# Optimization experiments

Hardware: AMD Instinct MI355X
Metric: run time of the kernel (lower is better)

Reference implementation:

```python
import jax, jax.numpy as jnp
import numpy as np
from jax import lax

N = 16384
K = 16
EPS = 1e-5


def setup_inputs() -> dict:
    key = jax.random.key(0)
    ks = jax.random.split(key, 10)

    def w(k, shape):
        fan_in = shape[0]
        return jax.random.normal(k, shape, jnp.float32) / np.sqrt(fan_in)

    return {
        "pos": jax.random.normal(ks[0], (N, 3), jnp.float32),
        "normal": jax.random.normal(ks[1], (N, 3), jnp.float32),
        # conv1 mlp: Linear(9,64) -> GroupNorm(8,64) -> ReLU -> Linear(64,64)
        "W1a": w(ks[2], (9, 64)), "b1a": jnp.zeros((64,), jnp.float32),
        "g1": jnp.ones((64,), jnp.float32), "beta1": jnp.zeros((64,), jnp.float32),
        "W1b": w(ks[3], (64, 64)), "b1b": jnp.zeros((64,), jnp.float32),
        # conv2 mlp: Linear(67,64) -> GroupNorm(8,64) -> ReLU -> Linear(64,64)
        "W2a": w(ks[4], (67, 64)), "b2a": jnp.zeros((64,), jnp.float32),
        "g2": jnp.ones((64,), jnp.float32), "beta2": jnp.zeros((64,), jnp.float32),
        "W2b": w(ks[5], (64, 64)), "b2b": jnp.zeros((64,), jnp.float32),
        # conv3 mlp: Linear(67,128) -> GroupNorm(16,128) -> ReLU -> Linear(128,128)
        "W3a": w(ks[6], (67, 128)), "b3a": jnp.zeros((128,), jnp.float32),
        "g3": jnp.ones((128,), jnp.float32), "beta3": jnp.zeros((128,), jnp.float32),
        "W3b": w(ks[7], (128, 128)), "b3b": jnp.zeros((128,), jnp.float32),
    }


def knn_graph(pos, k):
    # [N,N] squared distances; loop=True -> self is included (distance 0).
    sq = jnp.sum(pos * pos, axis=1)
    d2 = sq[:, None] + sq[None, :] - 2.0 * (pos @ pos.T)
    _, nbr = lax.top_k(-d2, k)  # [N,k] neighbor (source) indices per target node
    return nbr


def group_norm(h, gamma, beta, groups):
    # h: [N,k,C]; normalize each group of channels per edge sample.
    n, k, c = h.shape
    hg = h.reshape(n, k, groups, c // groups)
    mu = hg.mean(axis=-1, keepdims=True)
    var = hg.var(axis=-1, keepdims=True)
    hg = (hg - mu) * lax.rsqrt(var + EPS)
    return hg.reshape(n, k, c) * gamma + beta


def pointnet_conv(x, pos, nbr, Wa, ba, gamma, beta, Wb, bb, groups):
    # message: concat(x_j, pos_j - pos_i), MLP per edge, max-aggregate over neighbors
    xj = x[nbr]                              # [N,k,C_in]
    rel = pos[nbr] - pos[:, None, :]         # [N,k,3]
    m = jnp.concatenate([xj, rel], axis=-1)  # [N,k,C_in+3]
    h = m @ Wa + ba
    h = jax.nn.relu(group_norm(h, gamma, beta, groups))
    h = h @ Wb + bb
    return jnp.max(h, axis=1)                # [N,C_out]


def reference(pos, normal, W1a, b1a, g1, beta1, W1b, b1b,
              W2a, b2a, g2, beta2, W2b, b2b,
              W3a, b3a, g3, beta3, W3b, b3b):
    nbr = knn_graph(pos, K)
    h = jnp.concatenate([pos, normal], axis=-1)  # [N,6]
    h1 = jax.nn.relu(pointnet_conv(h, pos, nbr, W1a, b1a, g1, beta1, W1b, b1b, 8))
    h2 = jax.nn.relu(pointnet_conv(h1, pos, nbr, W2a, b2a, g2, beta2, W2b, b2b, 8))
    h3 = jax.nn.relu(pointnet_conv(h2, pos, nbr, W3a, b3a, g3, beta3, W3b, b3b, 16))
    return (h1, h2, h3)
```

## Files before the change

kernel.cpp:

```cpp
#include <hip/hip_runtime.h>
#include <hip/hip_bf16.h>
#include <stdint.h>

typedef unsigned long long u64;
typedef unsigned int u32;
typedef __attribute__((ext_vector_type(8))) short bf16x8;
typedef __attribute__((ext_vector_type(4))) float f32x4;

__device__ __forceinline__ float ldv(const void* p, size_t idx, int mode) {
  return mode ? __bfloat162float(((const __hip_bfloat16*)p)[idx])
              : ((const float*)p)[idx];
}
__device__ __forceinline__ void stv(void* p, size_t idx, int mode, float v) {
  if (mode) ((__hip_bfloat16*)p)[idx] = __float2bfloat16(v);
  else      ((float*)p)[idx] = v;
}
__device__ __forceinline__ unsigned short f2bfb(float f) {
  u32 u = __float_as_uint(f);
  u32 r = u + 0x7fffu + ((u >> 16) & 1u);
  return (unsigned short)(r >> 16);
}
__device__ __forceinline__ u64 shfl64(u64 v, int src) {
  int lo = __shfl((int)(u32)(v & 0xffffffffu), src, 64);
  int hi = __shfl((int)(u32)(v >> 32), src, 64);
  return ((u64)(u32)hi << 32) | (u32)lo;
}
__device__ __forceinline__ u64 shflxor64(u64 v, int m) {
  int lo = __shfl_xor((int)(u32)(v & 0xffffffffu), m, 64);
  int hi = __shfl_xor((int)(u32)(v >> 32), m, 64);
  return ((u64)(u32)hi << 32) | (u32)lo;
}
__device__ __forceinline__ u64 shfl64w16(u64 v, int src) {
  int lo = __shfl((int)(u32)(v & 0xffffffffu), src, 16);
  int hi = __shfl((int)(u32)(v >> 32), src, 16);
  return ((u64)(u32)hi << 32) | (u32)lo;
}

__global__ void PointNetSimple_61409442398998_kernel() {}

struct CvtEnt { const void* src; float* dst; int n; };
struct CvtArgs { CvtEnt e[12]; };
struct WEnt { const void* src; unsigned short* dst; int K, N, Kpad; };
struct WArgs { WEnt e[6]; };

__global__ void setup_kernel(const void* __restrict__ pos,
                             const void* __restrict__ nrm,
                             WArgs wa, CvtArgs ca,
                             int* __restrict__ flag,
                             float4* __restrict__ pos4,
                             float* __restrict__ h0, int n) {
  const unsigned short* u16p = (const unsigned short*)pos;
  int cnt = 0;
  for (int k = 0; k < 32; ++k) {
    int e = (u16p[k] >> 7) & 0xff;
    if (e >= 110 && e <= 140) cnt++;
  }
  const int mode = (cnt >= 26) ? 1 : 0;

  const int nprep = n >> 8;
  const int b = blockIdx.x;
  if (b < nprep) {
    int i = b * 256 + threadIdx.x;
    float x = ldv(pos, 3*(size_t)i+0, mode);
    float y = ldv(pos, 3*(size_t)i+1, mode);
    float z = ldv(pos, 3*(size_t)i+2, mode);
    pos4[i] = make_float4(x, y, z, x*x + y*y + z*z);
    h0[6*(size_t)i+0] = x; h0[6*(size_t)i+1] = y; h0[6*(size_t)i+2] = z;
    h0[6*(size_t)i+3] = ldv(nrm, 3*(size_t)i+0, mode);
    h0[6*(size_t)i+4] = ldv(nrm, 3*(size_t)i+1, mode);
    h0[6*(size_t)i+5] = ldv(nrm, 3*(size_t)i+2, mode);
  } else {
    int r = b - nprep;
    if (r < 6) {
      WEnt ent = wa.e[r];
      for (int t = threadIdx.x; t < ent.N * ent.Kpad; t += blockDim.x) {
        int nn = t / ent.Kpad;
        int k  = t - nn * ent.Kpad;
        float v = (k < ent.K) ? ldv(ent.src, (size_t)k * ent.N + nn, mode) : 0.0f;
        ent.dst[t] = f2bfb(v);
      }
      if (r == 0 && threadIdx.x == 0) flag[0] = mode;
    } else {
      for (int t2 = 0; t2 < 12; ++t2) {
        CvtEnt ent = ca.e[t2];
        for (int t = threadIdx.x; t < ent.n; t += blockDim.x)
          ent.dst[t] = ldv(ent.src, t, mode);
      }
    }
  }
}

#define KNN_TPB 512
#define KNN_WPB 8
#define KNN_TPW 4
#define KCH 1024

__device__ __forceinline__ void knn_flush(u64* __restrict__ wbuf_t, int& cnt,
                                          u64& val, float& th, int lane) {
  u64 cand = (lane < cnt) ? wbuf_t[lane] : ~0ull;
#pragma unroll
  for (int k = 2; k <= 64; k <<= 1) {
#pragma unroll
    for (int j = k >> 1; j > 0; j >>= 1) {
      u64 other = shflxor64(cand, j);
      bool up    = ((lane & k) == 0) || (k == 64);
      bool lower = ((lane & j) == 0);
      bool keepMin = (up == lower);
      u64 mn = cand < other ? cand : other;
      u64 mx = cand < other ? other : cand;
      cand = keepMin ? mn : mx;
    }
  }
  u64 rev = shfl64w16(cand, 15 - (lane & 15));
  u64 lo = val < rev ? val : rev;
#pragma unroll
  for (int j = 8; j > 0; j >>= 1) {
    u64 other = shflxor64(lo, j);
    bool lower = ((lane & j) == 0);
    u64 mn = lo < other ? lo : other;
    u64 mx = lo < other ? other : lo;
    lo = lower ? mn : mx;
  }
  val = (lane < 16) ? lo : ~0ull;
  u64 t15 = shfl64(val, 15);
  th = __uint_as_float((u32)(t15 >> 32));
  cnt = 0;
}

__global__ __launch_bounds__(KNN_TPB) void knn6_kernel(
    const float4* __restrict__ pos4, int* __restrict__ nbr, int n) {
  __shared__ float4 sp[2][KCH];
  __shared__ u64 buf[KNN_WPB][KNN_TPW][64];
  const int tid  = threadIdx.x;
  const int lane = tid & 63;
  const int wid  = tid >> 6;
  const int tbase = (blockIdx.x * KNN_WPB + wid) * KNN_TPW;

  float4 pi[KNN_TPW];
  float  thr[KNN_TPW];
  u64    val[KNN_TPW];
  int    cnt[KNN_TPW];
#pragma unroll
  for (int tt = 0; tt < KNN_TPW; ++tt) {
    pi[tt]  = pos4[tbase + tt];
    thr[tt] = 3.4e38f;
    val[tt] = ~0ull;
    cnt[tt] = 0;
  }

  for (int t = tid; t < KCH; t += KNN_TPB) sp[0][t] = pos4[t];
  __syncthreads();

  const int nch = n / KCH;
  for (int c = 0; c < nch; ++c) {
    const int cur = c & 1;
    float4 pre0, pre1;
    const bool more = (c + 1 < nch);
    if (more) {
      pre0 = pos4[(size_t)(c+1)*KCH + tid];
      pre1 = pos4[(size_t)(c+1)*KCH + KNN_TPB + tid];
    }
    for (int t = 0; t < KCH; t += 64) {
      float4 a = sp[cur][t + lane];
      float d2v[KNN_TPW];
      bool  pass[KNN_TPW];
#pragma unroll
      for (int tt = 0; tt < KNN_TPW; ++tt) {
        float d2 = (pi[tt].w + a.w)
                 - 2.0f*(pi[tt].x*a.x + pi[tt].y*a.y + pi[tt].z*a.z);
        d2 = fmaxf(d2, 0.0f);
        d2v[tt] = d2;
        pass[tt] = (d2 <= thr[tt]);
      }
      bool any = (pass[0] | pass[1]) | (pass[2] | pass[3]);
      if (__ballot(any) == 0ull) continue;

      const int base = c*KCH + t;
#pragma unroll
      for (int tt = 0; tt < KNN_TPW; ++tt) {
        u64 bal = __ballot(pass[tt]);
        if (bal) {
          int pc = __popcll(bal);
          if (cnt[tt] + pc > 64)
            knn_flush(&buf[wid][tt][0], cnt[tt], val[tt], thr[tt], lane);
          u32 mb = __builtin_amdgcn_mbcnt_lo((u32)bal, 0u);
          mb = __builtin_amdgcn_mbcnt_hi((u32)(bal >> 32), mb);
          if (pass[tt])
            buf[wid][tt][cnt[tt] + mb] =
                ((u64)__float_as_uint(d2v[tt]) << 32) | (u32)(base + lane);
          cnt[tt] += pc;
        }
      }
    }
    if (more) {
      sp[cur^1][tid] = pre0;
      sp[cur^1][KNN_TPB + tid] = pre1;
    }
    __syncthreads();
  }
#pragma unroll
  for (int tt = 0; tt < KNN_TPW; ++tt) {
    knn_flush(&buf[wid][tt][0], cnt[tt], val[tt], thr[tt], lane);
    if (lane < 16)
      nbr[(size_t)(tbase + tt)*16 + lane] = (int)(val[tt] & 0xffffffffu);
  }
}

template<int CIN, int CMID, int KT1, int NT, int KT2>
__global__ __launch_bounds__(256) void conv_mfma2_kernel(
    const float* __restrict__ xin,
    const float4* __restrict__ pos4,
    const int* __restrict__ nbr,
    const int* __restrict__ flag,
    const unsigned short* __restrict__ WaT,
    const unsigned short* __restrict__ WbT,
    const float* __restrict__ baf,
    const float* __restrict__ gmf,
    const float* __restrict__ btf,
    const float* __restrict__ bbf,
    float* __restrict__ xout,
    void* __restrict__ bout, size_t out_off)
{
  constexpr int K1PAD = KT1 * 32;
  constexpr int SB = CMID + 8;

  __shared__ unsigned short msgB[128 * SB];
  __shared__ float stage[4][32][20];

  const int tid  = threadIdx.x;
  const int lane = tid & 63;
  const int w    = tid >> 6;
  const int quad = lane >> 4;
  const int cl   = lane & 15;
  const int node0 = blockIdx.x * 8;
  const int mode = flag[0];

  bf16x8 afr[2][KT1];
#pragma unroll
  for (int mt = 0; mt < 2; ++mt) {
    const int node = node0 + w*2 + mt;
    const int j = nbr[(size_t)node*16 + cl];
    const float4 pin = pos4[node];
    const float4 pj = pos4[j];
    const float rx = pj.x - pin.x, ry = pj.y - pin.y, rz = pj.z - pin.z;
    if constexpr (CIN == 64) {
#pragma unroll
      for (int kt = 0; kt < 2; ++kt) {
        const float* p = &xin[(size_t)j*64 + kt*32 + quad*8];
        float4 a = *(const float4*)p;
        float4 b = *(const float4*)(p + 4);
        unsigned short o[8] = {f2bfb(a.x), f2bfb(a.y), f2bfb(a.z), f2bfb(a.w),
                               f2bfb(b.x), f2bfb(b.y), f2bfb(b.z), f2bfb(b.w)};
        afr[mt][kt] = *(bf16x8*)o;
      }
      unsigned short o[8] = {0,0,0,0,0,0,0,0};
      if (quad == 0) { o[0] = f2bfb(rx); o[1] = f2bfb(ry); o[2] = f2bfb(rz); }
      afr[mt][KT1-1] = *(bf16x8*)o;
    } else {
      unsigned short o[8] = {0,0,0,0,0,0,0,0};
      if (quad == 0) {
        const float* p = &xin[(size_t)j*6];
        o[0] = f2bfb(p[0]); o[1] = f2bfb(p[1]); o[2] = f2bfb(p[2]);
        o[3] = f2bfb(p[3]); o[4] = f2bfb(p[4]); o[5] = f2bfb(p[5]);
        o[6] = f2bfb(rx);   o[7] = f2bfb(ry);
      } else if (quad == 1) {
        o[0] = f2bfb(rz);
      }
      afr[mt][0] = *(bf16x8*)o;
    }
  }

  f32x4 acc1[2][NT];
#pragma unroll
  for (int mt = 0; mt < 2; ++mt)
#pragma unroll
    for (int nt = 0; nt < NT; ++nt) acc1[mt][nt] = (f32x4){0.f, 0.f, 0.f, 0.f};
#pragma unroll
  for (int kt = 0; kt < KT1; ++kt)
#pragma unroll
    for (int nt = 0; nt < NT; ++nt) {
      bf16x8 bfr = *(const bf16x8*)&WaT[(size_t)(nt*16 + cl) * K1PAD + kt*32 + quad*8];
      acc1[0][nt] = __builtin_amdgcn_mfma_f32_16x16x32_bf16(afr[0][kt], bfr, acc1[0][nt], 0, 0, 0);
      acc1[1][nt] = __builtin_amdgcn_mfma_f32_16x16x32_bf16(afr[1][kt], bfr, acc1[1][nt], 0, 0, 0);
    }

#pragma unroll
  for (int nt = 0; nt < NT; ++nt) {
    float bac = baf[nt*16 + cl];
#pragma unroll
    for (int mt = 0; mt < 2; ++mt)
#pragma unroll
      for (int reg = 0; reg < 4; ++reg)
        stage[w][mt*16 + quad*4 + reg][cl] = acc1[mt][nt][reg] + bac;
    asm volatile("" ::: "memory");
    {
      int row = lane >> 1, gl = lane & 1;
      float4 va = *(const float4*)&stage[w][row][gl*8];
      float4 vb = *(const float4*)&stage[w][row][gl*8 + 4];
      float s  = va.x+va.y+va.z+va.w + vb.x+vb.y+vb.z+vb.w;
      float q  = va.x*va.x+va.y*va.y+va.z*va.z+va.w*va.w
               + vb.x*vb.x+vb.y*vb.y+vb.z*vb.z+vb.w*vb.w;
      float mu = s * 0.125f;
      float var = q * 0.125f - mu * mu;
      float inv = rsqrtf(fmaxf(var, 0.0f) + 1e-5f);
      int cb = nt*16 + gl*8;
      float vv[8] = {va.x, va.y, va.z, va.w, vb.x, vb.y, vb.z, vb.w};
      unsigned short o[8];
#pragma unroll
      for (int e = 0; e < 8; ++e) {
        float t = (vv[e] - mu) * inv * gmf[cb+e] + btf[cb+e];
        o[e] = f2bfb(fmaxf(t, 0.0f));
      }
      *(bf16x8*)&msgB[(w*32 + row) * SB + cb] = *(bf16x8*)o;
    }
    asm volatile("" ::: "memory");
  }

  f32x4 acc2[2][NT];
#pragma unroll
  for (int mt = 0; mt < 2; ++mt)
#pragma unroll
    for (int nt = 0; nt < NT; ++nt) acc2[mt][nt] = (f32x4){0.f, 0.f, 0.f, 0.f};
#pragma unroll
  for (int kt = 0; kt < KT2; ++kt) {
    bf16x8 af0 = *(const bf16x8*)&msgB[(w*32 + cl)      * SB + kt*32 + quad*8];
    bf16x8 af1 = *(const bf16x8*)&msgB[(w*32 + 16 + cl) * SB + kt*32 + quad*8];
#pragma unroll
    for (int nt = 0; nt < NT; ++nt) {
      bf16x8 bfr = *(const bf16x8*)&WbT[(size_t)(nt*16 + cl) * CMID + kt*32 + quad*8];
      acc2[0][nt] = __builtin_amdgcn_mfma_f32_16x16x32_bf16(af0, bfr, acc2[0][nt], 0, 0, 0);
      acc2[1][nt] = __builtin_amdgcn_mfma_f32_16x16x32_bf16(af1, bfr, acc2[1][nt], 0, 0, 0);
    }
  }

#pragma unroll
  for (int mt = 0; mt < 2; ++mt) {
    int node = node0 + w*2 + mt;
#pragma unroll
    for (int nt = 0; nt < NT; ++nt) {
      float m = fmaxf(fmaxf(acc2[mt][nt][0], acc2[mt][nt][1]),
                      fmaxf(acc2[mt][nt][2], acc2[mt][nt][3]));
      m = fmaxf(m, __shfl_xor(m, 16, 64));
      m = fmaxf(m, __shfl_xor(m, 32, 64));
      float v = fmaxf(m + bbf[nt*16 + cl], 0.0f);
      if (quad == 0) {
        size_t oi = (size_t)node * CMID + nt*16 + cl;
        if (xout) xout[oi] = v;
        stv(bout, out_off + oi, mode, v);
      }
    }
  }
}

extern "C" void kernel_launch(void* const* d_in, const int* in_sizes, int n_in,
                              void* d_out, int out_size, void* d_ws, size_t ws_size,
                              hipStream_t stream) {
  (void)n_in; (void)ws_size; (void)in_sizes;
  int n = out_size / 256;
  if (n <= 0 || (n & 255)) n = 16384;

  float* ws = (float*)d_ws;
  int*    flag = (int*)ws;
  float4* pos4 = (float4*)(ws + 16);
  float*  h0   = ws + 16 + (size_t)4*n;
  float*  h1   = ws + 16 + (size_t)10*n;
  float*  h2   = ws + 16 + (size_t)74*n;
  int*    nbr  = (int*)(ws + 16 + (size_t)138*n);
  float*  vbuf = ws + 16 + (size_t)154*n;
  unsigned short* wtbuf = (unsigned short*)(vbuf + 1024);

  const int vsz[12] = {64,64,64,64, 64,64,64,64, 128,128,128,128};
  const int vsrc[12] = {3,4,5,7, 9,10,11,13, 15,16,17,19};
  CvtArgs ca;
  float* vptr[12];
  {
    int off = 0;
    for (int t = 0; t < 12; ++t) {
      ca.e[t].src = d_in[vsrc[t]];
      ca.e[t].dst = vbuf + off;
      ca.e[t].n   = vsz[t];
      vptr[t] = vbuf + off;
      off += vsz[t];
    }
  }
  const int wK[6]    = {9, 64, 67, 64, 67, 128};
  const int wN[6]    = {64, 64, 64, 64, 128, 128};
  const int wKp[6]   = {32, 64, 96, 64, 96, 128};
  const int wsrc[6]  = {2, 6, 8, 12, 14, 18};
  WArgs wa;
  unsigned short* wptr[6];
  {
    int off = 0;
    for (int t = 0; t < 6; ++t) {
      wa.e[t].src  = d_in[wsrc[t]];
      wa.e[t].dst  = wtbuf + off;
      wa.e[t].K    = wK[t];
      wa.e[t].N    = wN[t];
      wa.e[t].Kpad = wKp[t];
      wptr[t] = wtbuf + off;
      off += wN[t] * wKp[t];
    }
  }

  setup_kernel<<<n/256 + 7, 256, 0, stream>>>(
      d_in[0], d_in[1], wa, ca, flag, pos4, h0, n);
  knn6_kernel<<<n/(KNN_WPB*KNN_TPW), KNN_TPB, 0, stream>>>(pos4, nbr, n);

  conv_mfma2_kernel<6, 64, 1, 4, 2><<<n/8, 256, 0, stream>>>(
      h0, pos4, nbr, flag, wptr[0], wptr[1],
      vptr[0], vptr[1], vptr[2], vptr[3], h1, d_out, (size_t)0);
  conv_mfma2_kernel<64, 64, 3, 4, 2><<<n/8, 256, 0, stream>>>(
      h1, pos4, nbr, flag, wptr[2], wptr[3],
      vptr[4], vptr[5], vptr[6], vptr[7], h2, d_out, (size_t)n*64);
  conv_mfma2_kernel<64, 128, 3, 8, 4><<<n/8, 256, 0, stream>>>(
      h2, pos4, nbr, flag, wptr[4], wptr[5],
      vptr[8], vptr[9], vptr[10], vptr[11], (float*)nullptr, d_out, (size_t)n*128);
}
```

Before: 419.6 us.

## Seed kNN threshold from strided sample and halve targets per wave

Before the main scan, each wave evaluates 1024 strided sample points to set a tight 16th-nearest distance threshold per target. It then resets the candidate list but keeps that threshold, and the flush now takes the min with the existing threshold. The aim is to reject most points early and cut ballot, insert and flush work during the full scan. Targets per wave drop from 4 to 2, which gives more blocks but fewer distance evaluations per shared-memory load, and the inner loop is unrolled by 2.

New measurement: 396.4 us. -5.5%, faster.

```diff
diff --git a/kernel.cpp b/kernel.cpp
--- a/kernel.cpp
+++ b/kernel.cpp
@@ -92,7 +92,7 @@
 
 #define KNN_TPB 512
 #define KNN_WPB 8
-#define KNN_TPW 4
+#define KNN_TPW 2
 #define KCH 1024
 
 __device__ __forceinline__ void knn_flush(u64* __restrict__ wbuf_t, int& cnt,
@@ -123,11 +123,11 @@
   }
   val = (lane < 16) ? lo : ~0ull;
   u64 t15 = shfl64(val, 15);
-  th = __uint_as_float((u32)(t15 >> 32));
+  th = fminf(th, __uint_as_float((u32)(t15 >> 32)));
   cnt = 0;
 }
 
-__global__ __launch_bounds__(KNN_TPB) void knn6_kernel(
+__global__ __launch_bounds__(KNN_TPB) void knn7_kernel(
     const float4* __restrict__ pos4, int* __restrict__ nbr, int n) {
   __shared__ float4 sp[2][KCH];
   __shared__ u64 buf[KNN_WPB][KNN_TPW][64];
@@ -146,6 +146,39 @@
     thr[tt] = 3.4e38f;
     val[tt] = ~0ull;
     cnt[tt] = 0;
+  }
+
+  {
+    const int stride = n >> 4;
+    for (int s = 0; s < 16; ++s) {
+      float4 a = pos4[s*stride + lane];
+      const int base = s*stride;
+#pragma unroll
+      for (int tt = 0; tt < KNN_TPW; ++tt) {
+        float d2 = (pi[tt].w + a.w)
+                 - 2.0f*(pi[tt].x*a.x + pi[tt].y*a.y + pi[tt].z*a.z);
+        d2 = fmaxf(d2, 0.0f);
+        bool pass = (d2 <= thr[tt]);
+        u64 bal = __ballot(pass);
+        if (bal) {
+          int pc = __popcll(bal);
+          if (cnt[tt] + pc > 64)
+            knn_flush(&buf[wid][tt][0], cnt[tt], val[tt], thr[tt], lane);
+          u32 mb = __builtin_amdgcn_mbcnt_lo((u32)bal, 0u);
+          mb = __builtin_amdgcn_mbcnt_hi((u32)(bal >> 32), mb);
+          if (pass)
+            buf[wid][tt][cnt[tt] + mb] =
+                ((u64)__float_as_uint(d2) << 32) | (u32)(base + lane);
+          cnt[tt] += pc;
+        }
+      }
+    }
+#pragma unroll
+    for (int tt = 0; tt < KNN_TPW; ++tt) {
+      knn_flush(&buf[wid][tt][0], cnt[tt], val[tt], thr[tt], lane);
+      val[tt] = ~0ull;
+      cnt[tt] = 0;
+    }
   }
 
   for (int t = tid; t < KCH; t += KNN_TPB) sp[0][t] = pos4[t];
@@ -160,6 +193,7 @@
       pre0 = pos4[(size_t)(c+1)*KCH + tid];
       pre1 = pos4[(size_t)(c+1)*KCH + KNN_TPB + tid];
     }
+#pragma unroll 2
     for (int t = 0; t < KCH; t += 64) {
       float4 a = sp[cur][t + lane];
       float d2v[KNN_TPW];
@@ -172,23 +206,23 @@
         d2v[tt] = d2;
         pass[tt] = (d2 <= thr[tt]);
       }
-      bool any = (pass[0] | pass[1]) | (pass[2] | pass[3]);
-      if (__ballot(any) == 0ull) continue;
-
-      const int base = c*KCH + t;
-#pragma unroll
-      for (int tt = 0; tt < KNN_TPW; ++tt) {
-        u64 bal = __ballot(pass[tt]);
-        if (bal) {
-          int pc = __popcll(bal);
-          if (cnt[tt] + pc > 64)
-            knn_flush(&buf[wid][tt][0], cnt[tt], val[tt], thr[tt], lane);
-          u32 mb = __builtin_amdgcn_mbcnt_lo((u32)bal, 0u);
-          mb = __builtin_amdgcn_mbcnt_hi((u32)(bal >> 32), mb);
-          if (pass[tt])
-            buf[wid][tt][cnt[tt] + mb] =
-                ((u64)__float_as_uint(d2v[tt]) << 32) | (u32)(base + lane);
-          cnt[tt] += pc;
+      bool any = pass[0] | pass[1];
+      if (__ballot(any) != 0ull) {
+        const int base = c*KCH + t;
+#pragma unroll
+        for (int tt = 0; tt < KNN_TPW; ++tt) {
+          u64 bal = __ballot(pass[tt]);
+          if (bal) {
+            int pc = __popcll(bal);
+            if (cnt[tt] + pc > 64)
+              knn_flush(&buf[wid][tt][0], cnt[tt], val[tt], thr[tt], lane);
+            u32 mb = __builtin_amdgcn_mbcnt_lo((u32)bal, 0u);
+            mb = __builtin_amdgcn_mbcnt_hi((u32)(bal >> 32), mb);
+            if (pass[tt])
+              buf[wid][tt][cnt[tt] + mb] =
+                  ((u64)__float_as_uint(d2v[tt]) << 32) | (u32)(base + lane);
+            cnt[tt] += pc;
+          }
         }
       }
     }
@@ -404,7 +438,7 @@
 
   setup_kernel<<<n/256 + 7, 256, 0, stream>>>(
       d_in[0], d_in[1], wa, ca, flag, pos4, h0, n);
-  knn6_kernel<<<n/(KNN_WPB*KNN_TPW), KNN_TPB, 0, stream>>>(pos4, nbr, n);
+  knn7_kernel<<<n/(KNN_WPB*KNN_TPW), KNN_TPB, 0, stream>>>(pos4, nbr, n);
 
   conv_mfma2_kernel<6, 64, 1, 4, 2><<<n/8, 256, 0, stream>>>(
       h0, pos4, nbr, flag, wptr[0], wptr[1],
```
